# Optimization experiments

Hardware: AMD Instinct MI355X
Metric: run time of the kernel (lower is better)

The kernel has to match this reference:

```python
import jax, jax.numpy as jnp
import numpy as np

N = 100000  # nodes
IN, HID, OUT = 64, 64, 32  # in_channels, 2*out_channels, out_channels
E = 1600000  # edges (avg degree 16)


def _gcn_conv(x, src, dst, deg_inv_sqrt, W, b, n):
    # PyG GCNConv: h = X W ; out[dst] += norm * h[src] ; out += b
    h = x @ W  # [N, F_out]
    norm = (deg_inv_sqrt[src] * deg_inv_sqrt[dst])[:, None]  # [E+N, 1]
    msg = h[src] * norm  # gathered edge messages [E+N, F_out]
    return jax.ops.segment_sum(msg, dst, num_segments=n) + b


def setup_inputs() -> dict:
    key = jax.random.key(0)
    ks = jax.random.split(key, 6)
    x = jax.random.normal(ks[0], (N, IN), dtype=jnp.float32)
    edge_index = jax.random.randint(ks[1], (2, E), 0, N, dtype=jnp.int32)
    # glorot-ish init for the two GCN layers
    W1 = jax.random.normal(ks[2], (IN, HID), dtype=jnp.float32) * (1.0 / np.sqrt(IN))
    b1 = jnp.zeros((HID,), dtype=jnp.float32)
    W2 = jax.random.normal(ks[3], (HID, OUT), dtype=jnp.float32) * (1.0 / np.sqrt(HID))
    b2 = jnp.zeros((OUT,), dtype=jnp.float32)
    return {"x": x, "edge_index": edge_index, "W1": W1, "b1": b1, "W2": W2, "b2": b2}


def reference(x, edge_index, W1, b1, W2, b2):
    n = x.shape[0]
    loop = jnp.arange(n, dtype=edge_index.dtype)
    src = jnp.concatenate([edge_index[0], loop])  # add self-loops
    dst = jnp.concatenate([edge_index[1], loop])
    # symmetric degree normalization (deg includes self-loops, so deg >= 1)
    deg = jax.ops.segment_sum(jnp.ones(dst.shape[0], x.dtype), dst, num_segments=n)
    dis = jax.lax.rsqrt(deg)
    h = jax.nn.relu(_gcn_conv(x, src, dst, dis, W1, b1, n))
    out = jax.nn.relu(_gcn_conv(h, src, dst, dis, W2, b2, n))
    return out
```

## Files before the change

kernel.cpp:

```cpp
#include <hip/hip_runtime.h>


#define NBMAX 512

__device__ __forceinline__ unsigned bf16pair(float a, float b) {
  unsigned ua = __float_as_uint(a), ub = __float_as_uint(b);
  ua = (ua + 0x7fffu + ((ua >> 16) & 1u)) >> 16;
  ub = (ub + 0x7fffu + ((ub >> 16) & 1u)) >> 16;
  return ua | (ub << 16);
}
__device__ __forceinline__ float bf_lo(unsigned v) { return __uint_as_float(v << 16); }
__device__ __forceinline__ float bf_hi(unsigned v) { return __uint_as_float(v & 0xffff0000u); }


__global__ __launch_bounds__(256) void k_coarsehist(const int* __restrict__ dst,
                                                    int* __restrict__ ch,
                                                    int E, int NB) {
  __shared__ int lh[NBMAX];
  int t = threadIdx.x;
  lh[t] = 0; lh[t + 256] = 0;
  __syncthreads();
  for (int e = blockIdx.x * 256 + t; e < E; e += gridDim.x * 256)
    atomicAdd(&lh[dst[e] >> 8], 1);
  __syncthreads();
  for (int b = t; b < NB; b += 256) {
    int c = lh[b];
    if (c) atomicAdd(&ch[b], c);
  }
}

__global__ __launch_bounds__(512) void k_scanb(const int* __restrict__ ch,
                                               int* __restrict__ cbase,
                                               int* __restrict__ gcur,
                                               int* __restrict__ off,
                                               int NB, int n, int E) {
  __shared__ int lds[512];
  int t = threadIdx.x;
  int v = (t < NB) ? ch[t] : 0;
  lds[t] = v;
  __syncthreads();
  for (int d = 1; d < 512; d <<= 1) {
    int u = (t >= d) ? lds[t - d] : 0;
    __syncthreads();
    lds[t] += u;
    __syncthreads();
  }
  if (t < NB) {
    int exc = lds[t] - v;
    cbase[t] = exc;
    gcur[t]  = exc;
  }
  if (t == 0) off[n] = E;
}

__global__ __launch_bounds__(256) void k_binpairs(const int* __restrict__ src,
                                                  const int* __restrict__ dst,
                                                  int* __restrict__ gcur,
                                                  unsigned* __restrict__ pairs,
                                                  int E, int NB) {
  __shared__ int lcnt[NBMAX], gbase[NBMAX];
  int t = threadIdx.x;
  int tile0 = blockIdx.x * 4096;
  lcnt[t] = 0; lcnt[t + 256] = 0;
  __syncthreads();
#pragma unroll
  for (int j = 0; j < 16; ++j) {
    int e = tile0 + j * 256 + t;
    if (e < E) atomicAdd(&lcnt[dst[e] >> 8], 1);
  }
  __syncthreads();
  for (int b = t; b < NB; b += 256) {
    int c = lcnt[b];
    if (c) gbase[b] = atomicAdd(&gcur[b], c);
    lcnt[b] = 0;
  }
  __syncthreads();
#pragma unroll
  for (int j = 0; j < 16; ++j) {
    int e = tile0 + j * 256 + t;
    if (e < E) {
      int dv = dst[e];
      int b  = dv >> 8;
      int slot = atomicAdd(&lcnt[b], 1);
      pairs[gbase[b] + slot] = ((unsigned)src[e] << 8) | (unsigned)(dv & 255);
    }
  }
}

__global__ __launch_bounds__(256) void k_finesort(const unsigned* __restrict__ pairs,
                                                  const int* __restrict__ ch,
                                                  const int* __restrict__ cbase,
                                                  int* __restrict__ off,
                                                  float* __restrict__ dis,
                                                  int* __restrict__ ssrc, int n) {
  __shared__ int hist[256], lcur[256], wsum[4];
  __shared__ int sbuf[8192];
  int b = blockIdx.x;
  int node0 = b << 8;
  int nn = min(256, n - node0);
  int cnt = ch[b], base = cbase[b];
  int t = threadIdx.x;
  hist[t] = 0;
  __syncthreads();
  for (int e = t; e < cnt; e += 256)
    atomicAdd(&hist[pairs[base + e] & 255u], 1);
  __syncthreads();
  int c = hist[t];
  int lane = t & 63, wv = t >> 6;
  int inc = c;
#pragma unroll
  for (int d = 1; d < 64; d <<= 1) {
    int u = __shfl_up(inc, d);
    if (lane >= d) inc += u;
  }
  if (lane == 63) wsum[wv] = inc;
  __syncthreads();
  int pre = 0;
  for (int w = 0; w < wv; ++w) pre += wsum[w];
  int exc = pre + inc - c;
  if (t < nn) {
    off[node0 + t] = base + exc;
    dis[node0 + t] = rsqrtf((float)(c + 1));
  }
  lcur[t] = exc;
  __syncthreads();
  bool inlds = (cnt <= 8192);
  for (int e = t; e < cnt; e += 256) {
    unsigned p = pairs[base + e];
    int slot = atomicAdd(&lcur[p & 255u], 1);
    int sv = (int)(p >> 8);
    if (inlds) sbuf[slot] = sv;
    else       ssrc[base + slot] = sv;
  }
  __syncthreads();
  if (inlds)
    for (int e = t; e < cnt; e += 256) ssrc[base + e] = sbuf[e];
}


__device__ __forceinline__ int swz(int r, int q) {
  return r * 16 + (q ^ ((r >> 3) & 7));
}

__global__ __launch_bounds__(128) void k_gemm64t(const float* __restrict__ X,
                                                 const float* __restrict__ W,
                                                 const float* __restrict__ dis,
                                                 unsigned* __restrict__ Hb, int n) {
  __shared__ float4 Xl[128 * 16];
  __shared__ float4 Wl[64 * 16];
  int t = threadIdx.x;
  int row0 = blockIdx.x * 128;
#pragma unroll
  for (int j = 0; j < 8; ++j) Wl[t + j * 128] = ((const float4*)W)[t + j * 128];
#pragma unroll
  for (int j = 0; j < 16; ++j) {
    int v = t + j * 128;
    int r = v >> 4, q = v & 15;
    int gr = row0 + r;
    float4 val = (gr < n) ? ((const float4*)X)[(size_t)gr * 16 + q]
                          : make_float4(0.f, 0.f, 0.f, 0.f);
    Xl[swz(r, q)] = val;
  }
  __syncthreads();
  int tx = t & 7, ty = t >> 3;
  float acc[8][8];
#pragma unroll
  for (int i = 0; i < 8; ++i)
#pragma unroll
    for (int j = 0; j < 8; ++j) acc[i][j] = 0.f;
  int tysw = ty & 7;
  for (int kq = 0; kq < 16; ++kq) {
    float x_[8][4];
#pragma unroll
    for (int i = 0; i < 8; ++i) {
      float4 v = Xl[(ty * 8 + i) * 16 + (kq ^ tysw)];
      x_[i][0] = v.x; x_[i][1] = v.y; x_[i][2] = v.z; x_[i][3] = v.w;
    }
#pragma unroll
    for (int kk = 0; kk < 4; ++kk) {
      int k = kq * 4 + kk;
      float4 w0 = Wl[k * 16 + tx * 2];
      float4 w1 = Wl[k * 16 + tx * 2 + 1];
      float w_[8] = {w0.x, w0.y, w0.z, w0.w, w1.x, w1.y, w1.z, w1.w};
#pragma unroll
      for (int i = 0; i < 8; ++i)
#pragma unroll
        for (int j = 0; j < 8; ++j)
          acc[i][j] = fmaf(x_[i][kk], w_[j], acc[i][j]);
    }
  }
#pragma unroll
  for (int i = 0; i < 8; ++i) {
    int r = row0 + ty * 8 + i;
    if (r < n) {
      float d = dis[r];
      uint4 o;
      o.x = bf16pair(acc[i][0] * d, acc[i][1] * d);
      o.y = bf16pair(acc[i][2] * d, acc[i][3] * d);
      o.z = bf16pair(acc[i][4] * d, acc[i][5] * d);
      o.w = bf16pair(acc[i][6] * d, acc[i][7] * d);
      ((uint4*)Hb)[(size_t)r * 8 + tx] = o;
    }
  }
}

__global__ __launch_bounds__(128) void k_gemm32t(const float* __restrict__ P,
                                                 const float* __restrict__ W2,
                                                 const float* __restrict__ dis,
                                                 unsigned* __restrict__ Hb, int n) {
  __shared__ float4 Pl[128 * 16];
  __shared__ float4 Wl[64 * 8];
  int t = threadIdx.x;
  int row0 = blockIdx.x * 128;
#pragma unroll
  for (int j = 0; j < 4; ++j) Wl[t + j * 128] = ((const float4*)W2)[t + j * 128];
#pragma unroll
  for (int j = 0; j < 16; ++j) {
    int v = t + j * 128;
    int r = v >> 4, q = v & 15;
    int gr = row0 + r;
    float4 val = (gr < n) ? ((const float4*)P)[(size_t)gr * 16 + q]
                          : make_float4(0.f, 0.f, 0.f, 0.f);
    Pl[swz(r, q)] = val;
  }
  __syncthreads();
  int tx = t & 7, ty = t >> 3;
  float acc[8][4];
#pragma unroll
  for (int i = 0; i < 8; ++i)
#pragma unroll
    for (int j = 0; j < 4; ++j) acc[i][j] = 0.f;
  int tysw = ty & 7;
  for (int kq = 0; kq < 16; ++kq) {
    float x_[8][4];
#pragma unroll
    for (int i = 0; i < 8; ++i) {
      float4 v = Pl[(ty * 8 + i) * 16 + (kq ^ tysw)];
      x_[i][0] = v.x; x_[i][1] = v.y; x_[i][2] = v.z; x_[i][3] = v.w;
    }
#pragma unroll
    for (int kk = 0; kk < 4; ++kk) {
      int k = kq * 4 + kk;
      float4 w = Wl[k * 8 + tx];
      float w_[4] = {w.x, w.y, w.z, w.w};
#pragma unroll
      for (int i = 0; i < 8; ++i)
#pragma unroll
        for (int j = 0; j < 4; ++j)
          acc[i][j] = fmaf(x_[i][kk], w_[j], acc[i][j]);
    }
  }
#pragma unroll
  for (int i = 0; i < 8; ++i) {
    int r = row0 + ty * 8 + i;
    if (r < n) {
      float d = dis[r];
      uint2 o;
      o.x = bf16pair(acc[i][0] * d, acc[i][1] * d);
      o.y = bf16pair(acc[i][2] * d, acc[i][3] * d);
      ((uint2*)Hb)[(size_t)r * 8 + tx] = o;
    }
  }
}


__global__ __launch_bounds__(256) void k_gather64v(const int* __restrict__ off,
                                                   const int* __restrict__ ssrc,
                                                   const float* __restrict__ dis,
                                                   const uint2* __restrict__ Hb2,
                                                   const float* __restrict__ b1,
                                                   float* __restrict__ P, int n) {
  int lane = threadIdx.x & 63;
  int q = lane & 15, g = lane >> 4;
  int i = blockIdx.x * 4 + (threadIdx.x >> 6);
  if (i >= n) return;
  int beg = off[i], end = off[i + 1];
  float s0 = 0.f, s1 = 0.f, s2 = 0.f, s3 = 0.f;
  if (g == 0) {
    uint2 v = Hb2[(size_t)i * 16 + q];
    s0 = bf_lo(v.x); s1 = bf_hi(v.x); s2 = bf_lo(v.y); s3 = bf_hi(v.y);
  }
  int e = beg + g;
  for (; e + 4 < end; e += 8) {
    uint2 v0 = Hb2[(size_t)ssrc[e] * 16 + q];
    uint2 v1 = Hb2[(size_t)ssrc[e + 4] * 16 + q];
    s0 += bf_lo(v0.x) + bf_lo(v1.x);
    s1 += bf_hi(v0.x) + bf_hi(v1.x);
    s2 += bf_lo(v0.y) + bf_lo(v1.y);
    s3 += bf_hi(v0.y) + bf_hi(v1.y);
  }
  for (; e < end; e += 4) {
    uint2 v = Hb2[(size_t)ssrc[e] * 16 + q];
    s0 += bf_lo(v.x); s1 += bf_hi(v.x); s2 += bf_lo(v.y); s3 += bf_hi(v.y);
  }
  s0 += __shfl_xor(s0, 16); s1 += __shfl_xor(s1, 16);
  s2 += __shfl_xor(s2, 16); s3 += __shfl_xor(s3, 16);
  s0 += __shfl_xor(s0, 32); s1 += __shfl_xor(s1, 32);
  s2 += __shfl_xor(s2, 32); s3 += __shfl_xor(s3, 32);
  if (lane < 16) {
    float di = dis[i];
    float4 b = ((const float4*)b1)[q];
    float4 o;
    o.x = fmaxf(fmaf(di, s0, b.x), 0.f);
    o.y = fmaxf(fmaf(di, s1, b.y), 0.f);
    o.z = fmaxf(fmaf(di, s2, b.z), 0.f);
    o.w = fmaxf(fmaf(di, s3, b.w), 0.f);
    ((float4*)P)[(size_t)i * 16 + q] = o;
  }
}

__global__ __launch_bounds__(256) void k_gather32v(const int* __restrict__ off,
                                                   const int* __restrict__ ssrc,
                                                   const float* __restrict__ dis,
                                                   const uint2* __restrict__ Hb2,
                                                   const float* __restrict__ b2,
                                                   float* __restrict__ out, int n) {
  int lane = threadIdx.x & 63;
  int q = lane & 7, g = lane >> 3;
  int i = blockIdx.x * 4 + (threadIdx.x >> 6);
  if (i >= n) return;
  int beg = off[i], end = off[i + 1];
  float s0 = 0.f, s1 = 0.f, s2 = 0.f, s3 = 0.f;
  if (g == 0) {
    uint2 v = Hb2[(size_t)i * 8 + q];
    s0 = bf_lo(v.x); s1 = bf_hi(v.x); s2 = bf_lo(v.y); s3 = bf_hi(v.y);
  }
  int e = beg + g;
  for (; e + 8 < end; e += 16) {
    uint2 v0 = Hb2[(size_t)ssrc[e] * 8 + q];
    uint2 v1 = Hb2[(size_t)ssrc[e + 8] * 8 + q];
    s0 += bf_lo(v0.x) + bf_lo(v1.x);
    s1 += bf_hi(v0.x) + bf_hi(v1.x);
    s2 += bf_lo(v0.y) + bf_lo(v1.y);
    s3 += bf_hi(v0.y) + bf_hi(v1.y);
  }
  for (; e < end; e += 8) {
    uint2 v = Hb2[(size_t)ssrc[e] * 8 + q];
    s0 += bf_lo(v.x); s1 += bf_hi(v.x); s2 += bf_lo(v.y); s3 += bf_hi(v.y);
  }
  s0 += __shfl_xor(s0, 8);  s1 += __shfl_xor(s1, 8);
  s2 += __shfl_xor(s2, 8);  s3 += __shfl_xor(s3, 8);
  s0 += __shfl_xor(s0, 16); s1 += __shfl_xor(s1, 16);
  s2 += __shfl_xor(s2, 16); s3 += __shfl_xor(s3, 16);
  s0 += __shfl_xor(s0, 32); s1 += __shfl_xor(s1, 32);
  s2 += __shfl_xor(s2, 32); s3 += __shfl_xor(s3, 32);
  if (lane < 8) {
    float di = dis[i];
    float4 b = ((const float4*)b2)[q];
    float4 o;
    o.x = fmaxf(fmaf(di, s0, b.x), 0.f);
    o.y = fmaxf(fmaf(di, s1, b.y), 0.f);
    o.z = fmaxf(fmaf(di, s2, b.z), 0.f);
    o.w = fmaxf(fmaf(di, s3, b.w), 0.f);
    ((float4*)out)[(size_t)i * 8 + q] = o;
  }
}

extern "C" void kernel_launch(void* const* d_in, const int* in_sizes, int n_in,
                              void* d_out, int out_size, void* d_ws, size_t ws_size,
                              hipStream_t stream) {
  const float* x  = (const float*)d_in[0];
  const int*   ei = (const int*)d_in[1];
  const float* W1 = (const float*)d_in[2];
  const float* b1 = (const float*)d_in[3];
  const float* W2 = (const float*)d_in[4];
  const float* b2 = (const float*)d_in[5];
  float* out = (float*)d_out;

  const int n = in_sizes[0] / 64;
  const int E = in_sizes[1] / 2;
  const int* src = ei;
  const int* dst = ei + E;
  const int NB = (n + 255) >> 8;

  char* wp = (char*)d_ws;
  auto alloc = [&](size_t bytes) {
    char* p = wp;
    wp += (bytes + 15) & ~(size_t)15;
    return (void*)p;
  };
  unsigned* pairs = (unsigned*)alloc((size_t)E * 4);
  int*      ch    = (int*)alloc(NBMAX * 4);
  int*      cbase = (int*)alloc(NBMAX * 4);
  int*      gcur  = (int*)alloc(NBMAX * 4);
  int*      off   = (int*)alloc(((size_t)n + 1) * 4);
  float*    dis   = (float*)alloc((size_t)n * 4);
  int*      ssrc  = (int*)alloc((size_t)E * 4);
  unsigned* h1b   = (unsigned*)alloc((size_t)n * 64 * 2);
  float*    p1    = (float*)alloc((size_t)n * 64 * 4);
  unsigned* h2b   = (unsigned*)alloc((size_t)n * 32 * 2);

  auto cdiv = [](long long a, long long b) { return (unsigned)((a + b - 1) / b); };
  dim3 B(256);

  hipMemsetAsync(ch, 0, (size_t)NBMAX * 4, stream);
  k_coarsehist<<<512, B, 0, stream>>>(dst, ch, E, NB);
  k_scanb     <<<1, 512, 0, stream>>>(ch, cbase, gcur, off, NB, n, E);
  k_binpairs  <<<cdiv(E, 4096), B, 0, stream>>>(src, dst, gcur, pairs, E, NB);
  k_finesort  <<<NB, B, 0, stream>>>(pairs, ch, cbase, off, dis, ssrc, n);

  k_gemm64t   <<<cdiv(n, 128), 128, 0, stream>>>(x, W1, dis, h1b, n);
  k_gather64v <<<cdiv(n, 4), B, 0, stream>>>(off, ssrc, dis, (const uint2*)h1b, b1, p1, n);
  k_gemm32t   <<<cdiv(n, 128), 128, 0, stream>>>(p1, W2, dis, h2b, n);
  k_gather32v <<<cdiv(n, 4), B, 0, stream>>>(off, ssrc, dis, (const uint2*)h2b, b2, out, n);
}
```

Measured before the change: 203.0 us.

## Store layer-1 activations in bf16, unroll gathers deeper, enlarge binning tiles

The intermediate layer-1 output P is now written as packed bf16 instead of fp32, and the second GEMM unpacks it into fp32 in shared memory. This halves the traffic for that buffer. Both gather kernels are unrolled to four independent edge loads per iteration instead of two, to expose more memory-level parallelism. The edge-binning kernel processes 8192 edges per block instead of 4096, which reduces the number of global atomics on the bin cursors. The trade-off is extra rounding error from bf16 intermediates and higher register pressure in the gathers.

```diff
diff --git a/kernel.cpp b/kernel.cpp
--- a/kernel.cpp
+++ b/kernel.cpp
@@ -53,6 +53,7 @@
   if (t == 0) off[n] = E;
 }
 
+#define BIN_TILE 8192
 __global__ __launch_bounds__(256) void k_binpairs(const int* __restrict__ src,
                                                   const int* __restrict__ dst,
                                                   int* __restrict__ gcur,
@@ -60,11 +61,11 @@
                                                   int E, int NB) {
   __shared__ int lcnt[NBMAX], gbase[NBMAX];
   int t = threadIdx.x;
-  int tile0 = blockIdx.x * 4096;
+  int tile0 = blockIdx.x * BIN_TILE;
   lcnt[t] = 0; lcnt[t + 256] = 0;
   __syncthreads();
 #pragma unroll
-  for (int j = 0; j < 16; ++j) {
+  for (int j = 0; j < BIN_TILE / 256; ++j) {
     int e = tile0 + j * 256 + t;
     if (e < E) atomicAdd(&lcnt[dst[e] >> 8], 1);
   }
@@ -76,7 +77,7 @@
   }
   __syncthreads();
 #pragma unroll
-  for (int j = 0; j < 16; ++j) {
+  for (int j = 0; j < BIN_TILE / 256; ++j) {
     int e = tile0 + j * 256 + t;
     if (e < E) {
       int dv = dst[e];
@@ -204,7 +205,7 @@
   }
 }
 
-__global__ __launch_bounds__(128) void k_gemm32t(const float* __restrict__ P,
+__global__ __launch_bounds__(128) void k_gemm32t(const unsigned* __restrict__ Pb,
                                                  const float* __restrict__ W2,
                                                  const float* __restrict__ dis,
                                                  unsigned* __restrict__ Hb, int n) {
@@ -215,13 +216,16 @@
 #pragma unroll
   for (int j = 0; j < 4; ++j) Wl[t + j * 128] = ((const float4*)W2)[t + j * 128];
 #pragma unroll
-  for (int j = 0; j < 16; ++j) {
+  for (int j = 0; j < 8; ++j) {
     int v = t + j * 128;
-    int r = v >> 4, q = v & 15;
+    int r = v >> 3, u = v & 7;
     int gr = row0 + r;
-    float4 val = (gr < n) ? ((const float4*)P)[(size_t)gr * 16 + q]
-                          : make_float4(0.f, 0.f, 0.f, 0.f);
-    Pl[swz(r, q)] = val;
+    uint4 pv = (gr < n) ? ((const uint4*)Pb)[(size_t)gr * 8 + u]
+                        : make_uint4(0, 0, 0, 0);
+    float4 f0 = make_float4(bf_lo(pv.x), bf_hi(pv.x), bf_lo(pv.y), bf_hi(pv.y));
+    float4 f1 = make_float4(bf_lo(pv.z), bf_hi(pv.z), bf_lo(pv.w), bf_hi(pv.w));
+    Pl[swz(r, u * 2)]     = f0;
+    Pl[swz(r, u * 2 + 1)] = f1;
   }
   __syncthreads();
   int tx = t & 7, ty = t >> 3;
@@ -269,7 +273,7 @@
                                                    const float* __restrict__ dis,
                                                    const uint2* __restrict__ Hb2,
                                                    const float* __restrict__ b1,
-                                                   float* __restrict__ P, int n) {
+                                                   unsigned* __restrict__ Pb, int n) {
   int lane = threadIdx.x & 63;
   int q = lane & 15, g = lane >> 4;
   int i = blockIdx.x * 4 + (threadIdx.x >> 6);
@@ -281,13 +285,15 @@
     s0 = bf_lo(v.x); s1 = bf_hi(v.x); s2 = bf_lo(v.y); s3 = bf_hi(v.y);
   }
   int e = beg + g;
-  for (; e + 4 < end; e += 8) {
-    uint2 v0 = Hb2[(size_t)ssrc[e] * 16 + q];
-    uint2 v1 = Hb2[(size_t)ssrc[e + 4] * 16 + q];
-    s0 += bf_lo(v0.x) + bf_lo(v1.x);
-    s1 += bf_hi(v0.x) + bf_hi(v1.x);
-    s2 += bf_lo(v0.y) + bf_lo(v1.y);
-    s3 += bf_hi(v0.y) + bf_hi(v1.y);
+  for (; e + 12 < end; e += 16) {
+    uint2 v0 = Hb2[(size_t)ssrc[e]      * 16 + q];
+    uint2 v1 = Hb2[(size_t)ssrc[e + 4]  * 16 + q];
+    uint2 v2 = Hb2[(size_t)ssrc[e + 8]  * 16 + q];
+    uint2 v3 = Hb2[(size_t)ssrc[e + 12] * 16 + q];
+    s0 += bf_lo(v0.x) + bf_lo(v1.x) + bf_lo(v2.x) + bf_lo(v3.x);
+    s1 += bf_hi(v0.x) + bf_hi(v1.x) + bf_hi(v2.x) + bf_hi(v3.x);
+    s2 += bf_lo(v0.y) + bf_lo(v1.y) + bf_lo(v2.y) + bf_lo(v3.y);
+    s3 += bf_hi(v0.y) + bf_hi(v1.y) + bf_hi(v2.y) + bf_hi(v3.y);
   }
   for (; e < end; e += 4) {
     uint2 v = Hb2[(size_t)ssrc[e] * 16 + q];
@@ -300,12 +306,14 @@
   if (lane < 16) {
     float di = dis[i];
     float4 b = ((const float4*)b1)[q];
-    float4 o;
-    o.x = fmaxf(fmaf(di, s0, b.x), 0.f);
-    o.y = fmaxf(fmaf(di, s1, b.y), 0.f);
-    o.z = fmaxf(fmaf(di, s2, b.z), 0.f);
-    o.w = fmaxf(fmaf(di, s3, b.w), 0.f);
-    ((float4*)P)[(size_t)i * 16 + q] = o;
+    float o0 = fmaxf(fmaf(di, s0, b.x), 0.f);
+    float o1 = fmaxf(fmaf(di, s1, b.y), 0.f);
+    float o2 = fmaxf(fmaf(di, s2, b.z), 0.f);
+    float o3 = fmaxf(fmaf(di, s3, b.w), 0.f);
+    uint2 o;
+    o.x = bf16pair(o0, o1);
+    o.y = bf16pair(o2, o3);
+    ((uint2*)Pb)[(size_t)i * 16 + q] = o;
   }
 }
 
@@ -326,13 +334,15 @@
     s0 = bf_lo(v.x); s1 = bf_hi(v.x); s2 = bf_lo(v.y); s3 = bf_hi(v.y);
   }
   int e = beg + g;
-  for (; e + 8 < end; e += 16) {
-    uint2 v0 = Hb2[(size_t)ssrc[e] * 8 + q];
-    uint2 v1 = Hb2[(size_t)ssrc[e + 8] * 8 + q];
-    s0 += bf_lo(v0.x) + bf_lo(v1.x);
-    s1 += bf_hi(v0.x) + bf_hi(v1.x);
-    s2 += bf_lo(v0.y) + bf_lo(v1.y);
-    s3 += bf_hi(v0.y) + bf_hi(v1.y);
+  for (; e + 24 < end; e += 32) {
+    uint2 v0 = Hb2[(size_t)ssrc[e]      * 8 + q];
+    uint2 v1 = Hb2[(size_t)ssrc[e + 8]  * 8 + q];
+    uint2 v2 = Hb2[(size_t)ssrc[e + 16] * 8 + q];
+    uint2 v3 = Hb2[(size_t)ssrc[e + 24] * 8 + q];
+    s0 += bf_lo(v0.x) + bf_lo(v1.x) + bf_lo(v2.x) + bf_lo(v3.x);
+    s1 += bf_hi(v0.x) + bf_hi(v1.x) + bf_hi(v2.x) + bf_hi(v3.x);
+    s2 += bf_lo(v0.y) + bf_lo(v1.y) + bf_lo(v2.y) + bf_lo(v3.y);
+    s3 += bf_hi(v0.y) + bf_hi(v1.y) + bf_hi(v2.y) + bf_hi(v3.y);
   }
   for (; e < end; e += 8) {
     uint2 v = Hb2[(size_t)ssrc[e] * 8 + q];
@@ -387,7 +397,7 @@
   float*    dis   = (float*)alloc((size_t)n * 4);
   int*      ssrc  = (int*)alloc((size_t)E * 4);
   unsigned* h1b   = (unsigned*)alloc((size_t)n * 64 * 2);
-  float*    p1    = (float*)alloc((size_t)n * 64 * 4);
+  unsigned* p1b   = (unsigned*)alloc((size_t)n * 64 * 2);
   unsigned* h2b   = (unsigned*)alloc((size_t)n * 32 * 2);
 
   auto cdiv = [](long long a, long long b) { return (unsigned)((a + b - 1) / b); };
@@ -396,11 +406,11 @@
   hipMemsetAsync(ch, 0, (size_t)NBMAX * 4, stream);
   k_coarsehist<<<512, B, 0, stream>>>(dst, ch, E, NB);
   k_scanb     <<<1, 512, 0, stream>>>(ch, cbase, gcur, off, NB, n, E);
-  k_binpairs  <<<cdiv(E, 4096), B, 0, stream>>>(src, dst, gcur, pairs, E, NB);
+  k_binpairs  <<<cdiv(E, BIN_TILE), B, 0, stream>>>(src, dst, gcur, pairs, E, NB);
   k_finesort  <<<NB, B, 0, stream>>>(pairs, ch, cbase, off, dis, ssrc, n);
 
   k_gemm64t   <<<cdiv(n, 128), 128, 0, stream>>>(x, W1, dis, h1b, n);
-  k_gather64v <<<cdiv(n, 4), B, 0, stream>>>(off, ssrc, dis, (const uint2*)h1b, b1, p1, n);
-  k_gemm32t   <<<cdiv(n, 128), 128, 0, stream>>>(p1, W2, dis, h2b, n);
+  k_gather64v <<<cdiv(n, 4), B, 0, stream>>>(off, ssrc, dis, (const uint2*)h1b, b1, p1b, n);
+  k_gemm32t   <<<cdiv(n, 128), 128, 0, stream>>>(p1b, W2, dis, h2b, n);
   k_gather32v <<<cdiv(n, 4), B, 0, stream>>>(off, ssrc, dis, (const uint2*)h2b, b2, out, n);
 }
```

New measurement: 209.7 us. 1.03x slower.
